# Optimization experiments

Measured on AMD Instinct MI355X. Metric: run time of the kernel, lower is better.

The kernel has to match this reference:

```python
import jax, jax.numpy as jnp
import numpy as np
import math

D_MODEL = 1024
N_HEADS = 16
DEPTH = D_MODEL // N_HEADS
ROPE_BASE = 10000.0
LS_INIT = 1e-05


def _rope_cos_sin(seq_len, depth, dtype=jnp.float32):
    inv_freq = 1.0 / (ROPE_BASE ** (jnp.arange(0, depth, 2, dtype=jnp.float32) / depth))
    t = jnp.arange(seq_len, dtype=jnp.float32)
    freqs = jnp.einsum('i,j->ij', t, inv_freq)          # [S, depth/2]
    emb = jnp.concatenate([freqs, freqs], axis=-1)       # [S, depth]
    return emb.astype(dtype).cos()[None, None], emb.astype(dtype).sin()[None, None]  # wrong order fixed below


def rope_cos_sin(seq_len, depth):
    inv_freq = 1.0 / (ROPE_BASE ** (jnp.arange(0, depth, 2, dtype=jnp.float32) / depth))
    t = jnp.arange(seq_len, dtype=jnp.float32)
    freqs = jnp.einsum('i,j->ij', t, inv_freq)          # [S, depth/2]
    emb = jnp.concatenate([freqs, freqs], axis=-1)       # [S, depth]
    return jnp.cos(emb)[None, None], jnp.sin(emb)[None, None]  # [1,1,S,depth]


def rotate_half(x):
    x1, x2 = jnp.split(x, 2, axis=-1)
    return jnp.concatenate([-x2, x1], axis=-1)


def setup_inputs() -> dict:
    key = jax.random.key(0)
    ks = jax.random.split(key, 6)
    B, S, D = 2, 2048, D_MODEL
    s = 1.0 / math.sqrt(D)
    return {
        'query': jax.random.normal(ks[0], (B, S, D), dtype=jnp.float32),
        'Wq': jax.random.normal(ks[1], (D, D), dtype=jnp.float32) * s,
        'bq': jnp.zeros((D,), jnp.float32),
        'Wk': jax.random.normal(ks[2], (D, D), dtype=jnp.float32) * s,
        'bk': jnp.zeros((D,), jnp.float32),
        'Wv': jax.random.normal(ks[3], (D, D), dtype=jnp.float32) * s,
        'bv': jnp.zeros((D,), jnp.float32),
        'Wo': jax.random.normal(ks[4], (D, D), dtype=jnp.float32) * s,
        'bo': jnp.zeros((D,), jnp.float32),
        'gamma': jnp.full((D,), LS_INIT, jnp.float32),
    }


def reference(query, Wq, bq, Wk, bk, Wv, bv, Wo, bo, gamma):
    B, S, D = query.shape
    H, dh = N_HEADS, DEPTH

    def split_heads(x):  # [B,S,D] -> [B,H,S,dh]
        return x.reshape(B, S, H, dh).transpose(0, 2, 1, 3)

    # torch Linear: x @ W.T + b, W is [out,in]
    q = split_heads(query @ Wq.T + bq)
    k = split_heads(query @ Wk.T + bk)
    v = split_heads(query @ Wv.T + bv)

    cos, sin = rope_cos_sin(S, dh)  # [1,1,S,dh]
    q = q * cos + rotate_half(q) * sin
    k = k * cos + rotate_half(k) * sin

    logits = jnp.einsum('bhqd,bhkd->bhqk', q, k) / math.sqrt(dh)
    attn = jax.nn.softmax(logits, axis=-1)          # dropout = identity (eval)
    out = jnp.einsum('bhqk,bhkd->bhqd', attn, v)    # [B,H,S,dh]
    out = out.transpose(0, 2, 1, 3).reshape(B, S, D)
    out = out @ Wo.T + bo
    return gamma * out
```

## Files before the change

### kernel.cpp

```cpp
#include <hip/hip_runtime.h>
#include <hip/hip_bf16.h>
#include <math.h>

typedef __bf16 bf16_t;
typedef __bf16 bf16x8 __attribute__((ext_vector_type(8)));
typedef __bf16 bf16x4 __attribute__((ext_vector_type(4)));
typedef short short4v __attribute__((ext_vector_type(4)));
typedef float floatx4 __attribute__((ext_vector_type(4)));

#define SC_QK 0.18033688011112042f

__device__ __forceinline__ float fast_exp2(float x) {
#if __has_builtin(__builtin_amdgcn_exp2f)
  return __builtin_amdgcn_exp2f(x);
#else
  return exp2f(x);
#endif
}

__device__ __forceinline__ void async_load16(const bf16_t* g, bf16_t* l) {
  __builtin_amdgcn_global_load_lds(
      (__attribute__((address_space(1))) void*)(void*)g,
      (__attribute__((address_space(3))) void*)l, 16, 0, 0);
}

__device__ __forceinline__ floatx4 mfma_pv(bf16x4 vfrag, bf16x4 pfrag,
                                           floatx4 acc) {
#if __has_builtin(__builtin_amdgcn_mfma_f32_16x16x16bf16_1k)
  return __builtin_amdgcn_mfma_f32_16x16x16bf16_1k(
      __builtin_bit_cast(short4v, vfrag), __builtin_bit_cast(short4v, pfrag),
      acc, 0, 0, 0);
#else
  const bf16_t z = (bf16_t)0.0f;
  bf16x8 a = {vfrag[0], vfrag[1], vfrag[2], vfrag[3], z, z, z, z};
  bf16x8 b = {pfrag[0], pfrag[1], pfrag[2], pfrag[3], z, z, z, z};
  return __builtin_amdgcn_mfma_f32_16x16x32_bf16(a, b, acc, 0, 0, 0);
#endif
}

__global__ __launch_bounds__(256) void convert_kernel(
    const float* __restrict__ query, const float* __restrict__ Wq,
    const float* __restrict__ Wk, const float* __restrict__ Wv,
    const float* __restrict__ Wo, bf16_t* __restrict__ Xbf,
    bf16_t* __restrict__ Wqkv, bf16_t* __restrict__ Wobf) {
  long base = ((long)blockIdx.x * 256 + threadIdx.x) * 4;
  const float* src;
  bf16_t* dst;
  long off;
  if (base < 4194304L)      { src = query; dst = Xbf;             off = base; }
  else if (base < 5242880L) { src = Wq;    dst = Wqkv;            off = base - 4194304L; }
  else if (base < 6291456L) { src = Wk;    dst = Wqkv + 1048576;  off = base - 5242880L; }
  else if (base < 7340032L) { src = Wv;    dst = Wqkv + 2097152;  off = base - 6291456L; }
  else                      { src = Wo;    dst = Wobf;            off = base - 7340032L; }
  float4 v = *reinterpret_cast<const float4*>(src + off);
  dst[off + 0] = (bf16_t)v.x;
  dst[off + 1] = (bf16_t)v.y;
  dst[off + 2] = (bf16_t)v.z;
  dst[off + 3] = (bf16_t)v.w;
}

__global__ __launch_bounds__(256) void rope_tab_kernel(float* __restrict__ tab) {
  int idx = blockIdx.x * 256 + threadIdx.x;
  int s = idx >> 5;
  int p = idx & 31;
  float invf = __expf(-(float)p * 0.28782313662425576f);
  float ang = (float)s * invf;
  float c, sn;
  sincosf(ang, &sn, &c);
  tab[idx] = c;
  tab[65536 + idx] = sn;
}

__device__ __forceinline__ void gemm_tile_async(const bf16_t* __restrict__ A,
                                                const bf16_t* __restrict__ Bn,
                                                int m0, int n0,
                                                floatx4 acc[4][4]) {
  __shared__ __align__(16) bf16_t As[128 * 32];
  __shared__ __align__(16) bf16_t Bs[128 * 32];
  const int tid = threadIdx.x;
  const int lane = tid & 63;
  const int wave = tid >> 6;
  const int wm = (wave >> 1) * 64;
  const int wn = (wave & 1) * 64;
  const int lr = lane & 15;
  const int lq = lane >> 4;
  const int srow = lane >> 2;
  const int scol = (lane & 3) * 8;

  for (int kk = 0; kk < 1024; kk += 32) {
    __syncthreads();
#pragma unroll
    for (int u = 0; u < 2; u++) {
      int t = wave * 2 + u;
      int row = t * 16 + srow;
      async_load16(A + (size_t)(m0 + row) * 1024 + kk + scol, &As[t * 512]);
      async_load16(Bn + (size_t)(n0 + row) * 1024 + kk + scol, &Bs[t * 512]);
    }
    __syncthreads();
    bf16x8 af[4], bfr[4];
#pragma unroll
    for (int i = 0; i < 4; i++)
      af[i] = *reinterpret_cast<const bf16x8*>(&As[(wm + i * 16 + lr) * 32 + lq * 8]);
#pragma unroll
    for (int j = 0; j < 4; j++)
      bfr[j] = *reinterpret_cast<const bf16x8*>(&Bs[(wn + j * 16 + lr) * 32 + lq * 8]);
#pragma unroll
    for (int i = 0; i < 4; i++)
#pragma unroll
      for (int j = 0; j < 4; j++)
        acc[i][j] = __builtin_amdgcn_mfma_f32_16x16x32_bf16(af[i], bfr[j],
                                                            acc[i][j], 0, 0, 0);
  }
}

__global__ __launch_bounds__(256, 3) void qkv_kernel(
    const bf16_t* __restrict__ Xbf, const bf16_t* __restrict__ Wqkv,
    const float* __restrict__ bq, const float* __restrict__ bk,
    const float* __restrict__ bv, const float* __restrict__ Tab,
    bf16_t* __restrict__ Qbuf, bf16_t* __restrict__ Kbuf,
    bf16_t* __restrict__ Vt) {
  const int m0 = blockIdx.x * 128;
  const int n0 = blockIdx.y * 128;
  const int z = blockIdx.z;
  floatx4 acc[4][4];
  floatx4 zero4 = {0.f, 0.f, 0.f, 0.f};
#pragma unroll
  for (int i = 0; i < 4; i++)
#pragma unroll
    for (int j = 0; j < 4; j++) acc[i][j] = zero4;

  gemm_tile_async(Xbf, Wqkv + (size_t)z * 1048576, m0, n0, acc);

  const int lane = threadIdx.x & 63;
  const int wave = threadIdx.x >> 6;
  const int wm = (wave >> 1) * 64;
  const int wn = (wave & 1) * 64;
  const int lr = lane & 15;
  const int lq = lane >> 4;
  const int h = (n0 + wn) >> 6;

  if (z == 2) {
#pragma unroll
    for (int i = 0; i < 4; i++)
#pragma unroll
      for (int j = 0; j < 4; j++)
#pragma unroll
        for (int r = 0; r < 4; r++) {
          int m = m0 + wm + i * 16 + lq * 4 + r;
          int n = n0 + wn + j * 16 + lr;
          float v = acc[i][j][r] + bv[n];
          int b = m >> 11, s = m & 2047;
          int d = n & 63;
          Vt[((size_t)(b * 16 + h) * 64 + d) * 2048 + s] = (bf16_t)v;
        }
  } else {
    bf16_t* dst = (z == 0) ? Qbuf : Kbuf;
    const float* bias = (z == 0) ? bq : bk;
    const float sc = (z == 0) ? SC_QK : 1.0f;
#pragma unroll
    for (int i = 0; i < 4; i++)
#pragma unroll
      for (int r = 0; r < 4; r++) {
        int m = m0 + wm + i * 16 + lq * 4 + r;
        int b = m >> 11, s = m & 2047;
        size_t rowbase = ((size_t)(b * 16 + h) * 2048 + s) * 64;
#pragma unroll
        for (int jj = 0; jj < 2; jj++) {
          int d1 = jj * 16 + lr;
          int n1 = n0 + wn + d1;
          float x1 = acc[i][jj][r] + bias[n1];
          float x2 = acc[i][jj + 2][r] + bias[n1 + 32];
          float c = Tab[s * 32 + d1];
          float sn = Tab[65536 + s * 32 + d1];
          dst[rowbase + d1]      = (bf16_t)((x1 * c - x2 * sn) * sc);
          dst[rowbase + d1 + 32] = (bf16_t)((x2 * c + x1 * sn) * sc);
        }
      }
  }
}

__global__ __launch_bounds__(256, 3) void attn_kernel(
    const bf16_t* __restrict__ Qbuf, const bf16_t* __restrict__ Kbuf,
    const bf16_t* __restrict__ Vt, bf16_t* __restrict__ Ctx) {
  __shared__ __align__(16) bf16_t Sh[16384];
  bf16_t* Ks = Sh;
  bf16_t* Vs = Sh + 8192;
  const int tid = threadIdx.x;
  const int lane = tid & 63;
  const int w = tid >> 6;
  const int lr = lane & 15;
  const int lq = lane >> 4;
  const int q0 = blockIdx.x * 128;
  const int bh = blockIdx.y;
  const size_t hb = (size_t)bh * (2048 * 64);
  const int qw = q0 + w * 32;

  bf16x8 qf[2][2];
#pragma unroll
  for (int g = 0; g < 2; g++) {
    const bf16_t* qp = Qbuf + hb + (size_t)(qw + g * 16 + lr) * 64 + lq * 8;
    qf[g][0] = *reinterpret_cast<const bf16x8*>(qp);
    qf[g][1] = *reinterpret_cast<const bf16x8*>(qp + 32);
  }

  floatx4 o[2][4];
  float mr[2], lsum[2];
  floatx4 zero4 = {0.f, 0.f, 0.f, 0.f};
#pragma unroll
  for (int g = 0; g < 2; g++) {
    mr[g] = -1e30f;
    lsum[g] = 0.f;
#pragma unroll
    for (int dt = 0; dt < 4; dt++) o[g][dt] = zero4;
  }

  const int ksr = lane >> 3;
  const int ksb = lane & 7;
  const int vsr = lane >> 4;
  const int vsb = lane & 15;

  for (int kt = 0; kt < 16; kt++) {
    const int k0 = kt * 128;
    __syncthreads();
#pragma unroll
    for (int u = 0; u < 4; u++) {
      int t = w * 4 + u;
      {
        int r = t * 8 + ksr;
        int c = ksb ^ (r & 7);
        async_load16(Kbuf + hb + (size_t)(k0 + r) * 64 + c * 8, Ks + t * 512);
      }
      {
        int d = t * 4 + vsr;
        int c = vsb ^ (d & 15);
        async_load16(Vt + hb + (size_t)d * 2048 + k0 + c * 8, Vs + t * 512);
      }
    }
    __syncthreads();

    floatx4 sf[2][8];
#pragma unroll
    for (int nt = 0; nt < 8; nt++) {
      int krow = nt * 16 + lr;
      bf16x8 kf0 = *reinterpret_cast<const bf16x8*>(
          &Ks[krow * 64 + (lq ^ (krow & 7)) * 8]);
      bf16x8 kf1 = *reinterpret_cast<const bf16x8*>(
          &Ks[krow * 64 + ((4 + lq) ^ (krow & 7)) * 8]);
#pragma unroll
      for (int g = 0; g < 2; g++) {
        floatx4 z4 = zero4;
        z4 = __builtin_amdgcn_mfma_f32_16x16x32_bf16(kf0, qf[g][0], z4, 0, 0, 0);
        z4 = __builtin_amdgcn_mfma_f32_16x16x32_bf16(kf1, qf[g][1], z4, 0, 0, 0);
        sf[g][nt] = z4;
      }
    }

    float mn_[2], al[2], ls[2];
#pragma unroll
    for (int g = 0; g < 2; g++) {
      floatx4 mv = sf[g][0];
#pragma unroll
      for (int nt = 1; nt < 8; nt++) {
#pragma unroll
        for (int r = 0; r < 4; r++) mv[r] = fmaxf(mv[r], sf[g][nt][r]);
      }
      float m = fmaxf(fmaxf(mv[0], mv[1]), fmaxf(mv[2], mv[3]));
      m = fmaxf(m, __shfl_xor(m, 16, 64));
      m = fmaxf(m, __shfl_xor(m, 32, 64));
      float mn = fmaxf(mr[g], m);
      al[g] = fast_exp2(mr[g] - mn);
      mr[g] = mn;
      mn_[g] = mn;
      ls[g] = 0.f;
#pragma unroll
      for (int dt = 0; dt < 4; dt++) o[g][dt] *= al[g];
    }

#pragma unroll
    for (int nt = 0; nt < 8; nt++) {
      bf16x4 vf[4];
#pragma unroll
      for (int dt = 0; dt < 4; dt++) {
        int d = dt * 16 + lr;
        int blk = (2 * nt + (lq >> 1)) ^ (d & 15);
        vf[dt] = *reinterpret_cast<const bf16x4*>(
            &Vs[d * 128 + blk * 8 + (lq & 1) * 4]);
      }
#pragma unroll
      for (int g = 0; g < 2; g++) {
        bf16x4 pg;
#pragma unroll
        for (int r = 0; r < 4; r++) {
          float pv = fast_exp2(sf[g][nt][r] - mn_[g]);
          ls[g] += pv;
          pg[r] = (bf16_t)pv;
        }
#pragma unroll
        for (int dt = 0; dt < 4; dt++)
          o[g][dt] = mfma_pv(vf[dt], pg, o[g][dt]);
      }
    }
#pragma unroll
    for (int g = 0; g < 2; g++) {
      float t = ls[g];
      t += __shfl_xor(t, 16, 64);
      t += __shfl_xor(t, 32, 64);
      lsum[g] = lsum[g] * al[g] + t;
    }
  }

  const int b = bh >> 4;
  const int h = bh & 15;
#pragma unroll
  for (int g = 0; g < 2; g++) {
    float inv_l = 1.0f / lsum[g];
    size_t rowb = ((size_t)(b * 2048 + qw + g * 16 + lr)) * 1024 + h * 64;
#pragma unroll
    for (int dt = 0; dt < 4; dt++) {
      bf16x4 pk;
#pragma unroll
      for (int r = 0; r < 4; r++) pk[r] = (bf16_t)(o[g][dt][r] * inv_l);
      *reinterpret_cast<bf16x4*>(&Ctx[rowb + dt * 16 + lq * 4]) = pk;
    }
  }
}

__global__ __launch_bounds__(256, 3) void oproj_kernel(
    const bf16_t* __restrict__ Ctx, const bf16_t* __restrict__ Wobf,
    const float* __restrict__ bo, const float* __restrict__ gamma,
    float* __restrict__ out) {
  const int m0 = blockIdx.x * 128;
  const int n0 = blockIdx.y * 128;
  floatx4 acc[4][4];
  floatx4 zero4 = {0.f, 0.f, 0.f, 0.f};
#pragma unroll
  for (int i = 0; i < 4; i++)
#pragma unroll
    for (int j = 0; j < 4; j++) acc[i][j] = zero4;

  gemm_tile_async(Ctx, Wobf, m0, n0, acc);

  const int lane = threadIdx.x & 63;
  const int wave = threadIdx.x >> 6;
  const int wm = (wave >> 1) * 64;
  const int wn = (wave & 1) * 64;
  const int lr = lane & 15;
  const int lq = lane >> 4;
#pragma unroll
  for (int i = 0; i < 4; i++)
#pragma unroll
    for (int j = 0; j < 4; j++)
#pragma unroll
      for (int r = 0; r < 4; r++) {
        int m = m0 + wm + i * 16 + lq * 4 + r;
        int n = n0 + wn + j * 16 + lr;
        out[(size_t)m * 1024 + n] = gamma[n] * (acc[i][j][r] + bo[n]);
      }
}

extern "C" void kernel_launch(void* const* d_in, const int* in_sizes, int n_in,
                              void* d_out, int out_size, void* d_ws,
                              size_t ws_size, hipStream_t stream) {
  const float* query = (const float*)d_in[0];
  const float* Wq = (const float*)d_in[1];
  const float* bq = (const float*)d_in[2];
  const float* Wk = (const float*)d_in[3];
  const float* bk = (const float*)d_in[4];
  const float* Wv = (const float*)d_in[5];
  const float* bv = (const float*)d_in[6];
  const float* Wo = (const float*)d_in[7];
  const float* bo = (const float*)d_in[8];
  const float* gamma = (const float*)d_in[9];
  float* out = (float*)d_out;

  char* ws = (char*)d_ws;
  bf16_t* Xbf  = (bf16_t*)(ws);
  bf16_t* Wqkv = (bf16_t*)(ws + (8ull << 20));
  bf16_t* Wobf = (bf16_t*)(ws + (14ull << 20));
  bf16_t* Qbuf = (bf16_t*)(ws + (16ull << 20));
  bf16_t* Kbuf = (bf16_t*)(ws + (24ull << 20));
  bf16_t* Vt   = (bf16_t*)(ws + (32ull << 20));
  bf16_t* Ctx  = (bf16_t*)(ws + (40ull << 20));
  float*  Tab  = (float*)(ws + (40ull << 20));

  rope_tab_kernel<<<dim3(256), dim3(256), 0, stream>>>(Tab);
  convert_kernel<<<dim3(8192), dim3(256), 0, stream>>>(query, Wq, Wk, Wv, Wo,
                                                       Xbf, Wqkv, Wobf);
  qkv_kernel<<<dim3(32, 8, 3), dim3(256), 0, stream>>>(Xbf, Wqkv, bq, bk, bv,
                                                       Tab, Qbuf, Kbuf, Vt);
  attn_kernel<<<dim3(16, 32), dim3(256), 0, stream>>>(Qbuf, Kbuf, Vt, Ctx);
  oproj_kernel<<<dim3(32, 8), dim3(256), 0, stream>>>(Ctx, Wobf, bo, gamma, out);
}
```

Baseline: 221.1 us.

## Split attention over key halves with merge kernel; vectorize V transpose stores

The attention kernel now splits the key sequence into two halves along a new grid z dimension, so twice as many blocks run. Each half writes unnormalized partial outputs plus its running max and sum, and a new merge kernel combines them into Ctx. The aim is better CU occupancy, since the old 512-block grid underfills the GPU, at the cost of extra partial-output traffic, an extra launch, and aliased workspace reuse. The V epilogue in the QKV kernel now packs four consecutive sequence elements into one bf16x4 store instead of scalar strided stores. The attention launch bound also rises to 4 blocks per CU.

```diff
diff --git a/kernel.cpp b/kernel.cpp
--- a/kernel.cpp
+++ b/kernel.cpp
@@ -140,19 +140,21 @@
   const int h = (n0 + wn) >> 6;
 
   if (z == 2) {
+    const int b = m0 >> 11;
+    const int sbase = (m0 & 2047) + wm + lq * 4;
 #pragma unroll
     for (int i = 0; i < 4; i++)
 #pragma unroll
-      for (int j = 0; j < 4; j++)
-#pragma unroll
-        for (int r = 0; r < 4; r++) {
-          int m = m0 + wm + i * 16 + lq * 4 + r;
-          int n = n0 + wn + j * 16 + lr;
-          float v = acc[i][j][r] + bv[n];
-          int b = m >> 11, s = m & 2047;
-          int d = n & 63;
-          Vt[((size_t)(b * 16 + h) * 64 + d) * 2048 + s] = (bf16_t)v;
-        }
+      for (int j = 0; j < 4; j++) {
+        int n = n0 + wn + j * 16 + lr;
+        int d = j * 16 + lr;
+        float bias = bv[n];
+        bf16x4 pk;
+#pragma unroll
+        for (int r = 0; r < 4; r++) pk[r] = (bf16_t)(acc[i][j][r] + bias);
+        *reinterpret_cast<bf16x4*>(
+            &Vt[((size_t)(b * 16 + h) * 64 + d) * 2048 + sbase + i * 16]) = pk;
+      }
   } else {
     bf16_t* dst = (z == 0) ? Qbuf : Kbuf;
     const float* bias = (z == 0) ? bq : bk;
@@ -179,9 +181,10 @@
   }
 }
 
-__global__ __launch_bounds__(256, 3) void attn_kernel(
+__global__ __launch_bounds__(256, 4) void attn_kernel(
     const bf16_t* __restrict__ Qbuf, const bf16_t* __restrict__ Kbuf,
-    const bf16_t* __restrict__ Vt, bf16_t* __restrict__ Ctx) {
+    const bf16_t* __restrict__ Vt, bf16_t* __restrict__ Op0,
+    bf16_t* __restrict__ Op1, float2* __restrict__ Ml) {
   __shared__ __align__(16) bf16_t Sh[16384];
   bf16_t* Ks = Sh;
   bf16_t* Vs = Sh + 8192;
@@ -192,6 +195,7 @@
   const int lq = lane >> 4;
   const int q0 = blockIdx.x * 128;
   const int bh = blockIdx.y;
+  const int z = blockIdx.z;
   const size_t hb = (size_t)bh * (2048 * 64);
   const int qw = q0 + w * 32;
 
@@ -219,7 +223,7 @@
   const int vsr = lane >> 4;
   const int vsb = lane & 15;
 
-  for (int kt = 0; kt < 16; kt++) {
+  for (int kt = z * 8; kt < z * 8 + 8; kt++) {
     const int k0 = kt * 128;
     __syncthreads();
 #pragma unroll
@@ -309,20 +313,45 @@
     }
   }
 
-  const int b = bh >> 4;
-  const int h = bh & 15;
+  bf16_t* Op = z ? Op1 : Op0;
 #pragma unroll
   for (int g = 0; g < 2; g++) {
-    float inv_l = 1.0f / lsum[g];
-    size_t rowb = ((size_t)(b * 2048 + qw + g * 16 + lr)) * 1024 + h * 64;
+    int q = qw + g * 16 + lr;
+    size_t rowb = ((size_t)bh * 2048 + q) * 64;
 #pragma unroll
     for (int dt = 0; dt < 4; dt++) {
       bf16x4 pk;
 #pragma unroll
-      for (int r = 0; r < 4; r++) pk[r] = (bf16_t)(o[g][dt][r] * inv_l);
-      *reinterpret_cast<bf16x4*>(&Ctx[rowb + dt * 16 + lq * 4]) = pk;
-    }
-  }
+      for (int r = 0; r < 4; r++) pk[r] = (bf16_t)o[g][dt][r];
+      *reinterpret_cast<bf16x4*>(&Op[rowb + dt * 16 + lq * 4]) = pk;
+    }
+    if (lq == 0) Ml[((size_t)(z * 32 + bh)) * 2048 + q] = {mr[g], lsum[g]};
+  }
+}
+
+__global__ __launch_bounds__(256) void merge_kernel(
+    const bf16_t* __restrict__ Op0, const bf16_t* __restrict__ Op1,
+    const float2* __restrict__ Ml, bf16_t* __restrict__ Ctx) {
+  int idx = blockIdx.x * 256 + threadIdx.x;
+  int dq = idx & 15;
+  int q = (idx >> 4) & 2047;
+  int bh = idx >> 15;
+  float2 ml0 = Ml[(size_t)bh * 2048 + q];
+  float2 ml1 = Ml[(size_t)(32 + bh) * 2048 + q];
+  float M = fmaxf(ml0.x, ml1.x);
+  float w0 = fast_exp2(ml0.x - M);
+  float w1 = fast_exp2(ml1.x - M);
+  float inv = 1.0f / (w0 * ml0.y + w1 * ml1.y);
+  size_t off = ((size_t)bh * 2048 + q) * 64 + dq * 4;
+  bf16x4 a = *reinterpret_cast<const bf16x4*>(&Op0[off]);
+  bf16x4 b = *reinterpret_cast<const bf16x4*>(&Op1[off]);
+  bf16x4 o;
+#pragma unroll
+  for (int r = 0; r < 4; r++)
+    o[r] = (bf16_t)((w0 * (float)a[r] + w1 * (float)b[r]) * inv);
+  int b_ = bh >> 4, h = bh & 15;
+  *reinterpret_cast<bf16x4*>(
+      &Ctx[((size_t)(b_ * 2048 + q)) * 1024 + h * 64 + dq * 4]) = o;
 }
 
 __global__ __launch_bounds__(256, 3) void oproj_kernel(
@@ -375,19 +404,24 @@
 
   char* ws = (char*)d_ws;
   bf16_t* Xbf  = (bf16_t*)(ws);
+  bf16_t* Op0  = (bf16_t*)(ws);
   bf16_t* Wqkv = (bf16_t*)(ws + (8ull << 20));
+  float2* Ml   = (float2*)(ws + (8ull << 20));
   bf16_t* Wobf = (bf16_t*)(ws + (14ull << 20));
   bf16_t* Qbuf = (bf16_t*)(ws + (16ull << 20));
+  bf16_t* Ctx  = (bf16_t*)(ws + (16ull << 20));
   bf16_t* Kbuf = (bf16_t*)(ws + (24ull << 20));
   bf16_t* Vt   = (bf16_t*)(ws + (32ull << 20));
-  bf16_t* Ctx  = (bf16_t*)(ws + (40ull << 20));
   float*  Tab  = (float*)(ws + (40ull << 20));
+  bf16_t* Op1  = (bf16_t*)(ws + (40ull << 20));
 
   rope_tab_kernel<<<dim3(256), dim3(256), 0, stream>>>(Tab);
   convert_kernel<<<dim3(8192), dim3(256), 0, stream>>>(query, Wq, Wk, Wv, Wo,
                                                        Xbf, Wqkv, Wobf);
   qkv_kernel<<<dim3(32, 8, 3), dim3(256), 0, stream>>>(Xbf, Wqkv, bq, bk, bv,
                                                        Tab, Qbuf, Kbuf, Vt);
-  attn_kernel<<<dim3(16, 32), dim3(256), 0, stream>>>(Qbuf, Kbuf, Vt, Ctx);
+  attn_kernel<<<dim3(16, 32, 2), dim3(256), 0, stream>>>(Qbuf, Kbuf, Vt, Op0,
+                                                         Op1, Ml);
+  merge_kernel<<<dim3(4096), dim3(256), 0, stream>>>(Op0, Op1, Ml, Ctx);
   oproj_kernel<<<dim3(32, 8), dim3(256), 0, stream>>>(Ctx, Wobf, bo, gamma, out);
 }
```

Result: slower. 246.7 us (+11.6%).

## Double-buffer K/V tiles in attention and vectorize V-transpose stores

Applied to the files above, without the earlier changes.

The attention kernel now keeps two shared-memory K/V buffers and issues the async global-to-LDS loads for the next tile before computing on the current one. A single waitcnt plus barrier per iteration replaces the two syncthreads, so load latency can overlap the MFMA work. This doubles LDS use to 64KB, and the launch bound drops from 3 to 2 blocks per CU, which lowers occupancy. Separately, the V-projection epilogue packs four consecutive sequence elements into one bf16x4 store instead of four scalar strided stores.

```diff
diff --git a/kernel.cpp b/kernel.cpp
--- a/kernel.cpp
+++ b/kernel.cpp
@@ -140,19 +140,21 @@
   const int h = (n0 + wn) >> 6;
 
   if (z == 2) {
+    const int b = m0 >> 11;
+    const int sbase = (m0 & 2047) + wm + lq * 4;
 #pragma unroll
     for (int i = 0; i < 4; i++)
 #pragma unroll
-      for (int j = 0; j < 4; j++)
-#pragma unroll
-        for (int r = 0; r < 4; r++) {
-          int m = m0 + wm + i * 16 + lq * 4 + r;
-          int n = n0 + wn + j * 16 + lr;
-          float v = acc[i][j][r] + bv[n];
-          int b = m >> 11, s = m & 2047;
-          int d = n & 63;
-          Vt[((size_t)(b * 16 + h) * 64 + d) * 2048 + s] = (bf16_t)v;
-        }
+      for (int j = 0; j < 4; j++) {
+        int n = n0 + wn + j * 16 + lr;
+        int d = j * 16 + lr;
+        float bias = bv[n];
+        bf16x4 pk;
+#pragma unroll
+        for (int r = 0; r < 4; r++) pk[r] = (bf16_t)(acc[i][j][r] + bias);
+        *reinterpret_cast<bf16x4*>(
+            &Vt[((size_t)(b * 16 + h) * 64 + d) * 2048 + sbase + i * 16]) = pk;
+      }
   } else {
     bf16_t* dst = (z == 0) ? Qbuf : Kbuf;
     const float* bias = (z == 0) ? bq : bk;
@@ -179,12 +181,10 @@
   }
 }
 
-__global__ __launch_bounds__(256, 3) void attn_kernel(
+__global__ __launch_bounds__(256, 2) void attn_kernel(
     const bf16_t* __restrict__ Qbuf, const bf16_t* __restrict__ Kbuf,
     const bf16_t* __restrict__ Vt, bf16_t* __restrict__ Ctx) {
-  __shared__ __align__(16) bf16_t Sh[16384];
-  bf16_t* Ks = Sh;
-  bf16_t* Vs = Sh + 8192;
+  __shared__ __align__(16) bf16_t Sh[2][16384];
   const int tid = threadIdx.x;
   const int lane = tid & 63;
   const int w = tid >> 6;
@@ -219,9 +219,10 @@
   const int vsr = lane >> 4;
   const int vsb = lane & 15;
 
-  for (int kt = 0; kt < 16; kt++) {
+  auto stage = [&](int kt, int p) {
     const int k0 = kt * 128;
-    __syncthreads();
+    bf16_t* Ks = Sh[p];
+    bf16_t* Vs = Sh[p] + 8192;
 #pragma unroll
     for (int u = 0; u < 4; u++) {
       int t = w * 4 + u;
@@ -236,7 +237,21 @@
         async_load16(Vt + hb + (size_t)d * 2048 + k0 + c * 8, Vs + t * 512);
       }
     }
-    __syncthreads();
+  };
+
+  stage(0, 0);
+
+  for (int kt = 0; kt < 16; kt++) {
+    const int p = kt & 1;
+    const bf16_t* Ks = Sh[p];
+    const bf16_t* Vs = Sh[p] + 8192;
+
+    asm volatile("" ::: "memory");
+    __builtin_amdgcn_s_waitcnt(0x0f70);
+    __builtin_amdgcn_s_barrier();
+    asm volatile("" ::: "memory");
+
+    if (kt < 15) stage(kt + 1, p ^ 1);
 
     floatx4 sf[2][8];
 #pragma unroll
```

New measurement: 206.2 us. 1.07x faster.
